# Performance work log

Hardware: AMD Instinct MI355X
Metric: run time of the kernel (lower is better)

The kernel has to match this reference:

```python
import jax, jax.numpy as jnp
import numpy as np

N_OBJ, N_PTS, K_NN = 8, 2048, 10
TOL_CONTACT = 0.01


def setup_inputs() -> dict:
    key = jax.random.key(0)
    k1, k2, k3 = jax.random.split(key, 3)
    # per-object sampled points: xyz + (unit) normals
    pts = jax.random.normal(k1, (N_OBJ, N_PTS, 6), dtype=jnp.float32)
    nrm = pts[..., 3:6]
    nrm = nrm / jnp.linalg.norm(nrm, axis=-1, keepdims=True)
    points = jnp.concatenate([pts[..., :3], nrm], axis=-1)
    # near-identity rigid-ish transforms (keeps inverse well conditioned)
    T_est = jnp.eye(4, dtype=jnp.float32)[None] + 0.05 * jax.random.normal(k2, (N_OBJ, 4, 4), dtype=jnp.float32)
    T_plane = jnp.eye(4, dtype=jnp.float32) + 0.05 * jax.random.normal(k3, (4, 4), dtype=jnp.float32)
    return {"points": points, "T_est": T_est, "T_plane": T_plane, "k": K_NN}


def reference(points, T_est, T_plane, k):
    # points: [N, P, 6] (xyz, normal), T_est: [N, 4, 4], T_plane: [4, 4]
    N = points.shape[0]
    M = jnp.linalg.inv(T_plane) @ T_est                      # [N,4,4]
    xyz = points[..., :3]
    x = jnp.einsum('nij,npj->npi', M[:, :3, :3], xyz) + M[:, None, :3, 3]  # [N,P,3] points in plane frame
    z = x[..., 2]                                            # plane signed distance [N,P]
    nrm = points[..., 3:6]                                   # normals (untransformed, as in source)

    # all-pairs squared distances: d2[b,o,p,q] = ||x[b,p] - x[o,q]||^2
    sq = jnp.sum(x * x, axis=-1)                             # [N,P]
    d2 = sq[:, None, :, None] + sq[None, :, None, :] - 2.0 * jnp.einsum('bpd,oqd->bopq', x, x)
    neg_d2, idx = jax.lax.top_k(-d2, k)                      # [N,N,P,k], nearest k in object o for query (b,p)
    dist = jnp.sqrt(jnp.maximum(-neg_d2, 0.0))               # [N,N,P,k]

    # gather nearest points / normals from source object o
    o_idx = jnp.arange(N)[None, :, None, None]               # broadcast over [N,N,P,k]
    near = x[o_idx, idx]                                     # [N,N,P,k,3]
    near_n = nrm[o_idx, idx]                                 # [N,N,P,k,3]

    grad = near - x[:, None, :, None, :]                     # [N,N,P,k,3]
    grad = grad / jnp.linalg.norm(grad, axis=-1, keepdims=True)
    insides = jnp.sum(near_n * grad, axis=-1) > 0            # [N,N,P,k]
    inside = jnp.sum(insides, axis=-1) > k * 0.8             # [N,N,P]

    d0 = dist[..., 0]                                        # nearest distance [N,N,P]
    d0 = jnp.where(inside, -d0, d0)
    self_mask = jnp.eye(N, dtype=bool)[:, :, None]           # exclude o == b
    d0 = jnp.where(self_mask, jnp.inf, d0)
    sd_other = jnp.min(d0, axis=1)                           # [N,P] min over other objects

    signed_distance = jnp.minimum(z, sd_other)               # [N,P]
    intersects = signed_distance < -TOL_CONTACT
    return signed_distance, intersects
```

## Files before the change

### kernel.cpp

```cpp
#include <hip/hip_runtime.h>
#include <cfloat>
#include <math.h>

#define N_OBJ 8
#define N_PTS 2048
#define KNN   10
#define TOLC  0.01f
#define TPB   256
#define NW    4
#define QC    (N_PTS / NW)
#define PC2   128
#define NCHUNK2 (N_PTS / PC2)

__device__ __forceinline__ unsigned int enc_f(float f) {
    unsigned int u = __float_as_uint(f);
    return (u & 0x80000000u) ? ~u : (u | 0x80000000u);
}
__device__ __forceinline__ float dec_f(unsigned int e) {
    unsigned int u = (e & 0x80000000u) ? (e & 0x7fffffffu) : ~e;
    return __uint_as_float(u);
}

__global__ void k_transform(const float* __restrict__ pts,
                            const float* __restrict__ T_est,
                            const float* __restrict__ T_plane,
                            float4* __restrict__ P4g,
                            float4* __restrict__ N4g,
                            unsigned int* __restrict__ SD) {
    int gid = blockIdx.x * blockDim.x + threadIdx.x;
    if (gid >= N_OBJ * N_PTS) return;
    int b = gid >> 11;

    double m[16];
#pragma unroll
    for (int i = 0; i < 16; i++) m[i] = (double)T_plane[i];
    double inv[16];
    inv[0]  =  m[5]*m[10]*m[15] - m[5]*m[11]*m[14] - m[9]*m[6]*m[15] + m[9]*m[7]*m[14] + m[13]*m[6]*m[11] - m[13]*m[7]*m[10];
    inv[4]  = -m[4]*m[10]*m[15] + m[4]*m[11]*m[14] + m[8]*m[6]*m[15] - m[8]*m[7]*m[14] - m[12]*m[6]*m[11] + m[12]*m[7]*m[10];
    inv[8]  =  m[4]*m[9]*m[15]  - m[4]*m[11]*m[13] - m[8]*m[5]*m[15] + m[8]*m[7]*m[13] + m[12]*m[5]*m[11] - m[12]*m[7]*m[9];
    inv[12] = -m[4]*m[9]*m[14]  + m[4]*m[10]*m[13] + m[8]*m[5]*m[14] - m[8]*m[6]*m[13] - m[12]*m[5]*m[10] + m[12]*m[6]*m[9];
    inv[1]  = -m[1]*m[10]*m[15] + m[1]*m[11]*m[14] + m[9]*m[2]*m[15] - m[9]*m[3]*m[14] - m[13]*m[2]*m[11] + m[13]*m[3]*m[10];
    inv[5]  =  m[0]*m[10]*m[15] - m[0]*m[11]*m[14] - m[8]*m[2]*m[15] + m[8]*m[3]*m[14] + m[12]*m[2]*m[11] - m[12]*m[3]*m[10];
    inv[9]  = -m[0]*m[9]*m[15]  + m[0]*m[11]*m[13] + m[8]*m[1]*m[15] - m[8]*m[3]*m[13] - m[12]*m[1]*m[11] + m[12]*m[3]*m[9];
    inv[13] =  m[0]*m[9]*m[14]  - m[0]*m[10]*m[13] - m[8]*m[1]*m[14] + m[8]*m[2]*m[13] + m[12]*m[1]*m[10] - m[12]*m[2]*m[9];
    inv[2]  =  m[1]*m[6]*m[15]  - m[1]*m[7]*m[14]  - m[5]*m[2]*m[15] + m[5]*m[3]*m[14] + m[13]*m[2]*m[7]  - m[13]*m[3]*m[6];
    inv[6]  = -m[0]*m[6]*m[15]  + m[0]*m[7]*m[14]  + m[4]*m[2]*m[15] - m[4]*m[3]*m[14] - m[12]*m[2]*m[7]  + m[12]*m[3]*m[6];
    inv[10] =  m[0]*m[5]*m[15]  - m[0]*m[7]*m[13]  - m[4]*m[1]*m[15] + m[4]*m[3]*m[13] + m[12]*m[1]*m[7]  - m[12]*m[3]*m[5];
    inv[14] = -m[0]*m[5]*m[14]  + m[0]*m[6]*m[13]  + m[4]*m[1]*m[14] - m[4]*m[2]*m[13] - m[12]*m[1]*m[6]  + m[12]*m[2]*m[5];
    inv[3]  = -m[1]*m[6]*m[11]  + m[1]*m[7]*m[10]  + m[5]*m[2]*m[11] - m[5]*m[3]*m[10] - m[9]*m[2]*m[7]   + m[9]*m[3]*m[6];
    inv[7]  =  m[0]*m[6]*m[11]  - m[0]*m[7]*m[10]  - m[4]*m[2]*m[11] + m[4]*m[3]*m[10] + m[8]*m[2]*m[7]   - m[8]*m[3]*m[6];
    inv[11] = -m[0]*m[5]*m[11]  + m[0]*m[7]*m[9]   + m[4]*m[1]*m[11] - m[4]*m[3]*m[9]  - m[8]*m[1]*m[7]   + m[8]*m[3]*m[5];
    inv[15] =  m[0]*m[5]*m[10]  - m[0]*m[6]*m[9]   - m[4]*m[1]*m[10] + m[4]*m[2]*m[9]  + m[8]*m[1]*m[6]   - m[8]*m[2]*m[5];
    double det  = m[0]*inv[0] + m[1]*inv[4] + m[2]*inv[8] + m[3]*inv[12];
    double rdet = 1.0 / det;

    const float* Te = T_est + b * 16;
    double M[12];
#pragma unroll
    for (int i = 0; i < 3; i++)
#pragma unroll
        for (int j = 0; j < 4; j++) {
            double s = 0.0;
#pragma unroll
            for (int kk = 0; kk < 4; kk++) s += inv[i*4+kk] * rdet * (double)Te[kk*4+j];
            M[i*4+j] = s;
        }

    const float* pp = pts + (size_t)gid * 6;
    double px = pp[0], py = pp[1], pz = pp[2];
    float nx = pp[3], ny = pp[4], nz = pp[5];
    float x = (float)(M[0]*px + M[1]*py + M[2]*pz  + M[3]);
    float y = (float)(M[4]*px + M[5]*py + M[6]*pz  + M[7]);
    float z = (float)(M[8]*px + M[9]*py + M[10]*pz + M[11]);
    float sq = fmaf(x, x, fmaf(y, y, z * z));
    float w  = fmaf(nx, x, fmaf(ny, y, nz * z));
    P4g[gid] = make_float4(x, y, z, sq);
    N4g[gid] = make_float4(nx, ny, nz, w);
    SD[gid]  = enc_f(z);
}

#define QB2(PX,PY,PZ,PW,NX,NY,NZ,NWW) \
  "v_mul_f32 %[t0], " PZ ", %[mz0]\n" \
  "v_mul_f32 %[t2], " PZ ", %[mz1]\n" \
  "v_fma_f32 %[t0], %[my0], " PY ", %[t0]\n" \
  "v_fma_f32 %[t2], %[my1], " PY ", %[t2]\n" \
  "v_fma_f32 %[t0], %[mx0], " PX ", %[t0]\n" \
  "v_fma_f32 %[t2], %[mx1], " PX ", %[t2]\n" \
  "v_add_f32 %[t0], " PW ", %[t0]\n" \
  "v_add_f32 %[t2], " PW ", %[t2]\n" \
  "v_mul_f32 %[t1], " NZ ", %[gz0]\n" \
  "v_mul_f32 %[t3], " NZ ", %[gz1]\n" \
  "v_fma_f32 %[t1], %[gy0], " NY ", %[t1]\n" \
  "v_fma_f32 %[t3], %[gy1], " NY ", %[t3]\n" \
  "v_fma_f32 %[t1], %[gx0], " NX ", %[t1]\n" \
  "v_fma_f32 %[t3], %[gx1], " NX ", %[t3]\n" \
  "v_add_f32 %[t1], " NWW ", %[t1]\n" \
  "v_add_f32 %[t3], " NWW ", %[t3]\n" \
  "v_and_b32 %[t0], -2, %[t0]\n" \
  "v_and_b32 %[t2], -2, %[t2]\n" \
  "v_cmp_lt_f32 vcc, 0, %[t1]\n" \
  "v_cndmask_b32_e64 %[t1], 0, 1, vcc\n" \
  "v_or_b32 %[t0], %[t0], %[t1]\n" \
  "v_cmp_lt_f32 vcc, 0, %[t3]\n" \
  "v_cndmask_b32_e64 %[t3], 0, 1, vcc\n" \
  "v_or_b32 %[t2], %[t2], %[t3]\n" \
  "v_med3_f32 %[d9], %[d8], %[d9], %[t0]\n" \
  "v_med3_f32 %[d8], %[d7], %[d8], %[t0]\n" \
  "v_med3_f32 %[d7], %[d6], %[d7], %[t0]\n" \
  "v_med3_f32 %[d6], %[d5], %[d6], %[t0]\n" \
  "v_med3_f32 %[d5], %[d4], %[d5], %[t0]\n" \
  "v_med3_f32 %[d4], %[d3], %[d4], %[t0]\n" \
  "v_med3_f32 %[d3], %[d2], %[d3], %[t0]\n" \
  "v_med3_f32 %[d2], %[d1], %[d2], %[t0]\n" \
  "v_med3_f32 %[d1], %[d0], %[d1], %[t0]\n" \
  "v_min_f32 %[d0], %[d0], %[t0]\n" \
  "v_med3_f32 %[e9], %[e8], %[e9], %[t2]\n" \
  "v_med3_f32 %[e8], %[e7], %[e8], %[t2]\n" \
  "v_med3_f32 %[e7], %[e6], %[e7], %[t2]\n" \
  "v_med3_f32 %[e6], %[e5], %[e6], %[t2]\n" \
  "v_med3_f32 %[e5], %[e4], %[e5], %[t2]\n" \
  "v_med3_f32 %[e4], %[e3], %[e4], %[t2]\n" \
  "v_med3_f32 %[e3], %[e2], %[e3], %[t2]\n" \
  "v_med3_f32 %[e2], %[e1], %[e2], %[t2]\n" \
  "v_med3_f32 %[e1], %[e0], %[e1], %[t2]\n" \
  "v_min_f32 %[e0], %[e0], %[t2]\n"

__global__ void __launch_bounds__(TPB, 7) k_pairs(const float4* __restrict__ P4g,
                                                  const float4* __restrict__ N4g,
                                                  unsigned int* __restrict__ SD) {
    __shared__ float MRG[NW][PC2][KNN + 1];

    int bx    = blockIdx.x;
    int pair  = bx >> 4;
    int chunk = bx & (NCHUNK2 - 1);
    int b  = pair / 7;
    int oi = pair % 7;
    int o  = oi + (oi >= b ? 1 : 0);
    int tid  = threadIdx.x;
    int lane = tid & 63;
    int wu   = __builtin_amdgcn_readfirstlane(tid >> 6);
    int p0   = chunk * PC2 + lane;
    int p1   = p0 + 64;

    float4 xp0 = P4g[b * N_PTS + p0];
    float4 xp1 = P4g[b * N_PTS + p1];
    float mx0 = -2.0f * xp0.x, my0 = -2.0f * xp0.y, mz0 = -2.0f * xp0.z;
    float gx0 = -xp0.x, gy0 = -xp0.y, gz0 = -xp0.z;
    float mx1 = -2.0f * xp1.x, my1 = -2.0f * xp1.y, mz1 = -2.0f * xp1.z;
    float gx1 = -xp1.x, gy1 = -xp1.y, gz1 = -xp1.z;

    const float4* Po = P4g + o * N_PTS + wu * QC;
    const float4* No = N4g + o * N_PTS + wu * QC;
    unsigned long long ap = (unsigned long long)(uintptr_t)Po;
    unsigned long long an = (unsigned long long)(uintptr_t)No;

    const float FMAXE = __uint_as_float(0x7F7FFFFEu);
    float d0_ = FMAXE, d1_ = FMAXE, d2_ = FMAXE, d3_ = FMAXE, d4_ = FMAXE;
    float d5_ = FMAXE, d6_ = FMAXE, d7_ = FMAXE, d8_ = FMAXE, d9_ = FMAXE;
    float e0_ = FMAXE, e1_ = FMAXE, e2_ = FMAXE, e3_ = FMAXE, e4_ = FMAXE;
    float e5_ = FMAXE, e6_ = FMAXE, e7_ = FMAXE, e8_ = FMAXE, e9_ = FMAXE;
    float t0, t1, t2, t3;

    asm volatile(
        "s_mov_b64 s[32:33], %[ap]\n"
        "s_mov_b64 s[34:35], %[an]\n"
        "s_load_dwordx16 s[36:51], s[32:33], 0x0\n"
        "s_load_dwordx16 s[52:67], s[34:35], 0x0\n"
        "s_mov_b32 s30, 0\n"
        "Lkp%=:\n"
        "s_waitcnt lgkmcnt(0)\n"
        "s_load_dwordx16 s[68:83], s[32:33], 0x40\n"
        "s_load_dwordx16 s[84:99], s[34:35], 0x40\n"
        QB2("s36","s37","s38","s39","s52","s53","s54","s55")
        QB2("s40","s41","s42","s43","s56","s57","s58","s59")
        QB2("s44","s45","s46","s47","s60","s61","s62","s63")
        QB2("s48","s49","s50","s51","s64","s65","s66","s67")
        "s_waitcnt lgkmcnt(0)\n"
        "s_load_dwordx16 s[36:51], s[32:33], 0x80\n"
        "s_load_dwordx16 s[52:67], s[34:35], 0x80\n"
        QB2("s68","s69","s70","s71","s84","s85","s86","s87")
        QB2("s72","s73","s74","s75","s88","s89","s90","s91")
        QB2("s76","s77","s78","s79","s92","s93","s94","s95")
        QB2("s80","s81","s82","s83","s96","s97","s98","s99")
        "s_add_u32 s32, s32, 0x80\n"
        "s_addc_u32 s33, s33, 0\n"
        "s_add_u32 s34, s34, 0x80\n"
        "s_addc_u32 s35, s35, 0\n"
        "s_add_u32 s30, s30, 1\n"
        "s_cmp_lt_u32 s30, 64\n"
        "s_cbranch_scc1 Lkp%=\n"
        "s_waitcnt lgkmcnt(0)\n"
        : [d0]"+v"(d0_), [d1]"+v"(d1_), [d2]"+v"(d2_), [d3]"+v"(d3_),
          [d4]"+v"(d4_), [d5]"+v"(d5_), [d6]"+v"(d6_), [d7]"+v"(d7_),
          [d8]"+v"(d8_), [d9]"+v"(d9_),
          [e0]"+v"(e0_), [e1]"+v"(e1_), [e2]"+v"(e2_), [e3]"+v"(e3_),
          [e4]"+v"(e4_), [e5]"+v"(e5_), [e6]"+v"(e6_), [e7]"+v"(e7_),
          [e8]"+v"(e8_), [e9]"+v"(e9_),
          [t0]"=&v"(t0), [t1]"=&v"(t1), [t2]"=&v"(t2), [t3]"=&v"(t3)
        : [mx0]"v"(mx0), [my0]"v"(my0), [mz0]"v"(mz0),
          [gx0]"v"(gx0), [gy0]"v"(gy0), [gz0]"v"(gz0),
          [mx1]"v"(mx1), [my1]"v"(my1), [mz1]"v"(mz1),
          [gx1]"v"(gx1), [gy1]"v"(gy1), [gz1]"v"(gz1),
          [ap]"s"(ap), [an]"s"(an)
        : "s30","s32","s33","s34","s35","s36","s37","s38","s39",
          "s40","s41","s42","s43","s44","s45","s46","s47","s48","s49",
          "s50","s51","s52","s53","s54","s55","s56","s57","s58","s59",
          "s60","s61","s62","s63","s64","s65","s66","s67","s68","s69",
          "s70","s71","s72","s73","s74","s75","s76","s77","s78","s79",
          "s80","s81","s82","s83","s84","s85","s86","s87","s88","s89",
          "s90","s91","s92","s93","s94","s95","s96","s97","s98","s99",
          "scc","vcc","memory");

    float td0[KNN] = {d0_, d1_, d2_, d3_, d4_, d5_, d6_, d7_, d8_, d9_};
    float td1[KNN] = {e0_, e1_, e2_, e3_, e4_, e5_, e6_, e7_, e8_, e9_};

    if (wu > 0) {
#pragma unroll
        for (int j = 0; j < KNN; j++) {
            MRG[wu][lane][j]      = td0[j];
            MRG[wu][lane + 64][j] = td1[j];
        }
    }
    __syncthreads();

    if (wu == 0) {
#pragma unroll
        for (int ww = 1; ww < NW; ww++) {
#pragma unroll
            for (int j = 0; j < KNN; j++) {
                float cp = MRG[ww][lane][j];
#pragma unroll
                for (int t = KNN - 1; t >= 1; --t)
                    td0[t] = __builtin_amdgcn_fmed3f(td0[t - 1], td0[t], cp);
                td0[0] = fminf(td0[0], cp);
                float cq = MRG[ww][lane + 64][j];
#pragma unroll
                for (int t = KNN - 1; t >= 1; --t)
                    td1[t] = __builtin_amdgcn_fmed3f(td1[t - 1], td1[t], cq);
                td1[0] = fminf(td1[0], cq);
            }
        }

        int cnt0 = 0, cnt1 = 0;
#pragma unroll
        for (int j = 0; j < KNN; j++) {
            cnt0 += (int)(__float_as_uint(td0[j]) & 1u);
            cnt1 += (int)(__float_as_uint(td1[j]) & 1u);
        }
        float dd0 = __uint_as_float(__float_as_uint(td0[0]) & 0xFFFFFFFEu) + xp0.w;
        float r0  = sqrtf(fmaxf(dd0, 0.0f));
        if (cnt0 > 8) r0 = -r0;
        atomicMin(&SD[b * N_PTS + p0], enc_f(r0));
        float dd1 = __uint_as_float(__float_as_uint(td1[0]) & 0xFFFFFFFEu) + xp1.w;
        float r1  = sqrtf(fmaxf(dd1, 0.0f));
        if (cnt1 > 8) r1 = -r1;
        atomicMin(&SD[b * N_PTS + p1], enc_f(r1));
    }
}

__global__ void k_final(const unsigned int* __restrict__ SD,
                       float* __restrict__ out) {
    int gid = blockIdx.x * blockDim.x + threadIdx.x;
    if (gid >= N_OBJ * N_PTS) return;
    float sd = dec_f(SD[gid]);
    out[gid] = sd;
    out[N_OBJ * N_PTS + gid] = (sd < -TOLC) ? 1.0f : 0.0f;
}

extern "C" void kernel_launch(void* const* d_in, const int* in_sizes, int n_in,
                              void* d_out, int out_size, void* d_ws, size_t ws_size,
                              hipStream_t stream) {
    const float* pts     = (const float*)d_in[0];
    const float* T_est   = (const float*)d_in[1];
    const float* T_plane = (const float*)d_in[2];

    float4*       P4 = (float4*)d_ws;
    float4*       N4 = P4 + N_OBJ * N_PTS;
    unsigned int* SD = (unsigned int*)(N4 + N_OBJ * N_PTS);

    float* out = (float*)d_out;

    k_transform<<<(N_OBJ * N_PTS) / 256, 256, 0, stream>>>(pts, T_est, T_plane, P4, N4, SD);
    k_pairs<<<N_OBJ * (N_OBJ - 1) * NCHUNK2, TPB, 0, stream>>>(P4, N4, SD);
    k_final<<<(N_OBJ * N_PTS) / 256, 256, 0, stream>>>(SD, out);
}
```

Before: 178.5 us.

## Stage source-object points and normals in LDS instead of scalar-loading per wave

Each block now copies the full point and normal arrays of the source object into 64 KB of shared memory, then the inner loop streams candidates with double-buffered ds_read_b128 into VGPRs instead of s_load_dwordx16 into SGPRs. The aim is to take the scalar cache and constant-load latency out of the hot loop and let the wave overlap LDS reads with the med3 top-k updates. In exchange, each block pays a 64 KB global-to-LDS copy, the large LDS footprint and the 64 clobbered VGPRs cut occupancy (launch bounds drop from 7 to 2), and the merge buffer now aliases the staging area, which needs an extra barrier.

Measured after the change: 195.9 us. 1.1x slower.

```diff
diff --git a/kernel.cpp b/kernel.cpp
--- a/kernel.cpp
+++ b/kernel.cpp
@@ -125,10 +125,43 @@
   "v_med3_f32 %[e1], %[e0], %[e1], %[t2]\n" \
   "v_min_f32 %[e0], %[e0], %[t2]\n"
 
-__global__ void __launch_bounds__(TPB, 7) k_pairs(const float4* __restrict__ P4g,
+#define RDA(O0,O1,O2,O3,NO0,NO1,NO2,NO3) \
+  "ds_read_b128 v[32:35], %[lb] offset:" O0 "\n" \
+  "ds_read_b128 v[36:39], %[lb] offset:" O1 "\n" \
+  "ds_read_b128 v[40:43], %[lb] offset:" O2 "\n" \
+  "ds_read_b128 v[44:47], %[lb] offset:" O3 "\n" \
+  "ds_read_b128 v[48:51], %[lb] offset:" NO0 "\n" \
+  "ds_read_b128 v[52:55], %[lb] offset:" NO1 "\n" \
+  "ds_read_b128 v[56:59], %[lb] offset:" NO2 "\n" \
+  "ds_read_b128 v[60:63], %[lb] offset:" NO3 "\n"
+#define RDB(O0,O1,O2,O3,NO0,NO1,NO2,NO3) \
+  "ds_read_b128 v[64:67], %[lb] offset:" O0 "\n" \
+  "ds_read_b128 v[68:71], %[lb] offset:" O1 "\n" \
+  "ds_read_b128 v[72:75], %[lb] offset:" O2 "\n" \
+  "ds_read_b128 v[76:79], %[lb] offset:" O3 "\n" \
+  "ds_read_b128 v[80:83], %[lb] offset:" NO0 "\n" \
+  "ds_read_b128 v[84:87], %[lb] offset:" NO1 "\n" \
+  "ds_read_b128 v[88:91], %[lb] offset:" NO2 "\n" \
+  "ds_read_b128 v[92:95], %[lb] offset:" NO3 "\n"
+
+#define QBA \
+  QB2("v32","v33","v34","v35","v48","v49","v50","v51") \
+  QB2("v36","v37","v38","v39","v52","v53","v54","v55") \
+  QB2("v40","v41","v42","v43","v56","v57","v58","v59") \
+  QB2("v44","v45","v46","v47","v60","v61","v62","v63")
+#define QBB \
+  QB2("v64","v65","v66","v67","v80","v81","v82","v83") \
+  QB2("v68","v69","v70","v71","v84","v85","v86","v87") \
+  QB2("v72","v73","v74","v75","v88","v89","v90","v91") \
+  QB2("v76","v77","v78","v79","v92","v93","v94","v95")
+
+__global__ void __launch_bounds__(TPB, 2) k_pairs(const float4* __restrict__ P4g,
                                                   const float4* __restrict__ N4g,
                                                   unsigned int* __restrict__ SD) {
-    __shared__ float MRG[NW][PC2][KNN + 1];
+    __shared__ __align__(16) unsigned char shraw[2 * N_PTS * sizeof(float4)];
+    float4* Pl = (float4*)shraw;
+    float4* Nl = (float4*)(shraw + 32768);
+    float (*MRG)[PC2][KNN + 1] = (float (*)[PC2][KNN + 1])shraw;
 
     int bx    = blockIdx.x;
     int pair  = bx >> 4;
@@ -142,6 +175,11 @@
     int p0   = chunk * PC2 + lane;
     int p1   = p0 + 64;
 
+    for (int i = tid; i < N_PTS; i += TPB) {
+        Pl[i] = P4g[o * N_PTS + i];
+        Nl[i] = N4g[o * N_PTS + i];
+    }
+
     float4 xp0 = P4g[b * N_PTS + p0];
     float4 xp1 = P4g[b * N_PTS + p1];
     float mx0 = -2.0f * xp0.x, my0 = -2.0f * xp0.y, mz0 = -2.0f * xp0.z;
@@ -149,10 +187,7 @@
     float mx1 = -2.0f * xp1.x, my1 = -2.0f * xp1.y, mz1 = -2.0f * xp1.z;
     float gx1 = -xp1.x, gy1 = -xp1.y, gz1 = -xp1.z;
 
-    const float4* Po = P4g + o * N_PTS + wu * QC;
-    const float4* No = N4g + o * N_PTS + wu * QC;
-    unsigned long long ap = (unsigned long long)(uintptr_t)Po;
-    unsigned long long an = (unsigned long long)(uintptr_t)No;
+    unsigned int lb = (unsigned int)(uintptr_t)(&Pl[wu * QC]);
 
     const float FMAXE = __uint_as_float(0x7F7FFFFEu);
     float d0_ = FMAXE, d1_ = FMAXE, d2_ = FMAXE, d3_ = FMAXE, d4_ = FMAXE;
@@ -161,59 +196,54 @@
     float e5_ = FMAXE, e6_ = FMAXE, e7_ = FMAXE, e8_ = FMAXE, e9_ = FMAXE;
     float t0, t1, t2, t3;
 
+    __syncthreads();
+
     asm volatile(
-        "s_mov_b64 s[32:33], %[ap]\n"
-        "s_mov_b64 s[34:35], %[an]\n"
-        "s_load_dwordx16 s[36:51], s[32:33], 0x0\n"
-        "s_load_dwordx16 s[52:67], s[34:35], 0x0\n"
+        RDA("0","16","32","48","32768","32784","32800","32816")
         "s_mov_b32 s30, 0\n"
         "Lkp%=:\n"
+        RDB("64","80","96","112","32832","32848","32864","32880")
+        "s_waitcnt lgkmcnt(8)\n"
+        QBA
+        RDA("128","144","160","176","32896","32912","32928","32944")
+        "s_waitcnt lgkmcnt(8)\n"
+        QBB
+        "v_add_u32 %[lb], 128, %[lb]\n"
+        "s_add_u32 s30, s30, 1\n"
+        "s_cmp_lt_u32 s30, 63\n"
+        "s_cbranch_scc1 Lkp%=\n"
+        RDB("64","80","96","112","32832","32848","32864","32880")
+        "s_waitcnt lgkmcnt(8)\n"
+        QBA
         "s_waitcnt lgkmcnt(0)\n"
-        "s_load_dwordx16 s[68:83], s[32:33], 0x40\n"
-        "s_load_dwordx16 s[84:99], s[34:35], 0x40\n"
-        QB2("s36","s37","s38","s39","s52","s53","s54","s55")
-        QB2("s40","s41","s42","s43","s56","s57","s58","s59")
-        QB2("s44","s45","s46","s47","s60","s61","s62","s63")
-        QB2("s48","s49","s50","s51","s64","s65","s66","s67")
-        "s_waitcnt lgkmcnt(0)\n"
-        "s_load_dwordx16 s[36:51], s[32:33], 0x80\n"
-        "s_load_dwordx16 s[52:67], s[34:35], 0x80\n"
-        QB2("s68","s69","s70","s71","s84","s85","s86","s87")
-        QB2("s72","s73","s74","s75","s88","s89","s90","s91")
-        QB2("s76","s77","s78","s79","s92","s93","s94","s95")
-        QB2("s80","s81","s82","s83","s96","s97","s98","s99")
-        "s_add_u32 s32, s32, 0x80\n"
-        "s_addc_u32 s33, s33, 0\n"
-        "s_add_u32 s34, s34, 0x80\n"
-        "s_addc_u32 s35, s35, 0\n"
-        "s_add_u32 s30, s30, 1\n"
-        "s_cmp_lt_u32 s30, 64\n"
-        "s_cbranch_scc1 Lkp%=\n"
-        "s_waitcnt lgkmcnt(0)\n"
+        QBB
         : [d0]"+v"(d0_), [d1]"+v"(d1_), [d2]"+v"(d2_), [d3]"+v"(d3_),
           [d4]"+v"(d4_), [d5]"+v"(d5_), [d6]"+v"(d6_), [d7]"+v"(d7_),
           [d8]"+v"(d8_), [d9]"+v"(d9_),
           [e0]"+v"(e0_), [e1]"+v"(e1_), [e2]"+v"(e2_), [e3]"+v"(e3_),
           [e4]"+v"(e4_), [e5]"+v"(e5_), [e6]"+v"(e6_), [e7]"+v"(e7_),
           [e8]"+v"(e8_), [e9]"+v"(e9_),
-          [t0]"=&v"(t0), [t1]"=&v"(t1), [t2]"=&v"(t2), [t3]"=&v"(t3)
+          [t0]"=&v"(t0), [t1]"=&v"(t1), [t2]"=&v"(t2), [t3]"=&v"(t3),
+          [lb]"+v"(lb)
         : [mx0]"v"(mx0), [my0]"v"(my0), [mz0]"v"(mz0),
           [gx0]"v"(gx0), [gy0]"v"(gy0), [gz0]"v"(gz0),
           [mx1]"v"(mx1), [my1]"v"(my1), [mz1]"v"(mz1),
-          [gx1]"v"(gx1), [gy1]"v"(gy1), [gz1]"v"(gz1),
-          [ap]"s"(ap), [an]"s"(an)
-        : "s30","s32","s33","s34","s35","s36","s37","s38","s39",
-          "s40","s41","s42","s43","s44","s45","s46","s47","s48","s49",
-          "s50","s51","s52","s53","s54","s55","s56","s57","s58","s59",
-          "s60","s61","s62","s63","s64","s65","s66","s67","s68","s69",
-          "s70","s71","s72","s73","s74","s75","s76","s77","s78","s79",
-          "s80","s81","s82","s83","s84","s85","s86","s87","s88","s89",
-          "s90","s91","s92","s93","s94","s95","s96","s97","s98","s99",
+          [gx1]"v"(gx1), [gy1]"v"(gy1), [gz1]"v"(gz1)
+        : "s30",
+          "v32","v33","v34","v35","v36","v37","v38","v39",
+          "v40","v41","v42","v43","v44","v45","v46","v47",
+          "v48","v49","v50","v51","v52","v53","v54","v55",
+          "v56","v57","v58","v59","v60","v61","v62","v63",
+          "v64","v65","v66","v67","v68","v69","v70","v71",
+          "v72","v73","v74","v75","v76","v77","v78","v79",
+          "v80","v81","v82","v83","v84","v85","v86","v87",
+          "v88","v89","v90","v91","v92","v93","v94","v95",
           "scc","vcc","memory");
 
     float td0[KNN] = {d0_, d1_, d2_, d3_, d4_, d5_, d6_, d7_, d8_, d9_};
     float td1[KNN] = {e0_, e1_, e2_, e3_, e4_, e5_, e6_, e7_, e8_, e9_};
 
+    __syncthreads();
     if (wu > 0) {
 #pragma unroll
         for (int j = 0; j < KNN; j++) {
@@ -280,7 +310,7 @@
 
     float* out = (float*)d_out;
 
-    k_transform<<<(N_OBJ * N_PTS) / 256, 256, 0, stream>>>(pts, T_est, T_plane, P4, N4, SD);
+    k_transform<<<(N_OBJ * N_PTS) / TPB, TPB, 0, stream>>>(pts, T_est, T_plane, P4, N4, SD);
     k_pairs<<<N_OBJ * (N_OBJ - 1) * NCHUNK2, TPB, 0, stream>>>(P4, N4, SD);
-    k_final<<<(N_OBJ * N_PTS) / 256, 256, 0, stream>>>(SD, out);
-}
+    k_final<<<(N_OBJ * N_PTS) / TPB, TPB, 0, stream>>>(SD, out);
+}
```
